# Kernel tuning notes

Hardware: AMD Instinct MI355X
Metric: run time of the kernel (lower is better)

Reference implementation:

```python
import jax, jax.numpy as jnp
import numpy as np

B, S, D = 8, 2048, 256


def setup_inputs() -> dict:
    key = jax.random.key(0)
    ks = jax.random.split(key, 8)
    nodes = jax.random.normal(ks[0], (B, S, D), dtype=jnp.float32)
    mask = jax.random.randint(ks[1], (B, S), 0, 2, dtype=jnp.int32)
    # ensure at least one unmasked position per row to avoid all--inf softmax
    mask = mask.at[:, 0].set(1)
    scale = 1.0 / np.sqrt(D)
    Wq = jax.random.normal(ks[2], (D, D), dtype=jnp.float32) * scale
    bq = jnp.zeros((D,), dtype=jnp.float32)
    Wk = jax.random.normal(ks[3], (D, D), dtype=jnp.float32) * scale
    bk = jnp.zeros((D,), dtype=jnp.float32)
    Wv = jax.random.normal(ks[4], (D, D), dtype=jnp.float32) * scale
    bv = jnp.zeros((D,), dtype=jnp.float32)
    return {"nodes": nodes, "mask": mask, "Wq": Wq, "bq": bq,
            "Wk": Wk, "bk": bk, "Wv": Wv, "bv": bv}


def reference(nodes, mask, Wq, bq, Wk, bk, Wv, bv):
    # Linear layers: x @ W.T + b (torch nn.Linear convention)
    q = jnp.einsum('bsd,ed->bse', nodes, Wq) + bq   # [B,S,D]
    k = jnp.einsum('bsd,ed->bse', nodes, Wk) + bk
    v = jnp.einsum('bsd,ed->bse', nodes, Wv) + bv
    d = k.shape[-1]
    scores = jnp.einsum('bqd,bkd->bqk', q, k) / jnp.sqrt(jnp.float32(d))  # [B,S,S]
    # mask[b, j] == 0 masks key column j for every query row
    scores = jnp.where(mask[:, None, :] != 0, scores, -jnp.inf)
    attn = jax.nn.softmax(scores, axis=-1)           # [B,S,S]
    weighted = jnp.einsum('bqk,bkd->bqd', attn, v)   # [B,S,D]
    return jnp.mean(weighted, axis=1)                # [B,D]
```

## Files before the change

### kernel.cpp

```cpp
#include <hip/hip_runtime.h>
#include <hip/hip_bf16.h>
#include <stdint.h>


typedef short short8 __attribute__((ext_vector_type(8)));
typedef float floatx4 __attribute__((ext_vector_type(4)));
typedef float floatx2 __attribute__((ext_vector_type(2)));

#define MFMA16(a, b, c) __builtin_amdgcn_mfma_f32_16x16x32_bf16((a), (b), (c), 0, 0, 0)

#define ASYNC16(gsrc, ldst)                                                    \
    __builtin_amdgcn_global_load_lds(                                          \
        (__attribute__((address_space(1))) void*)(void*)(gsrc),                \
        (__attribute__((address_space(3))) void*)(ldst), 16, 0, 0)

static __device__ __forceinline__ unsigned short f2bf(float f) {
    union { float f; unsigned u; } v; v.f = f;
    unsigned r = v.u + 0x7fffu + ((v.u >> 16) & 1u);
    return (unsigned short)(r >> 16);
}
static __device__ __forceinline__ float bf2f(unsigned short h) {
    union { unsigned u; float f; } v; v.u = ((unsigned)h) << 16;
    return v.f;
}

__global__ __launch_bounds__(256) void k_cc(
    const float* __restrict__ nodes, const float* __restrict__ Wq,
    const float* __restrict__ Wk, const float* __restrict__ Wv,
    unsigned short* __restrict__ nbf, unsigned short* __restrict__ wbf,
    const int* __restrict__ mask, int* __restrict__ cidx, int* __restrict__ cnt,
    int* __restrict__ slot_of ,
    unsigned short* __restrict__ kbt,
    float* __restrict__ zbase ,
    float* __restrict__ outp )
{
    int blk = blockIdx.x;
    if (blk < 2144) {
        int unit = blk * 256 + threadIdx.x;
        const float* src;
        unsigned short* dst;
        int off;
        if (unit < 524288) {
            src = nodes; dst = nbf; off = unit * 8;
        } else {
            int j = (unit - 524288) * 8;
            int m = j >> 16;
            int r = j & 65535;
            src = (m == 0) ? Wq : (m == 1 ? Wk : Wv);
            dst = wbf + m * 65536;
            off = r;
        }
        float4 a = *(const float4*)(src + off);
        float4 b = *(const float4*)(src + off + 4);
        short8 o;
        o[0] = f2bf(a.x); o[1] = f2bf(a.y); o[2] = f2bf(a.z); o[3] = f2bf(a.w);
        o[4] = f2bf(b.x); o[5] = f2bf(b.y); o[6] = f2bf(b.z); o[7] = f2bf(b.w);
        *(short8*)(dst + off) = o;
        return;
    }
    if (blk < 2152) {
        if (threadIdx.x < 64) {
            int b = blk - 2144, lane = threadIdx.x;
            int base = 0;
            for (int c = 0; c < 2048; c += 64) {
                int m = mask[b * 2048 + c + lane];
                unsigned long long bal = __ballot(m != 0);
                int pre = __popcll(bal & ((1ull << lane) - 1ull));
                if (m) {
                    cidx[b * 2048 + base + pre] = c + lane;
                    slot_of[b * 2048 + c + lane] = base + pre;
                } else {
                    slot_of[b * 2048 + c + lane] = -1;
                }
                base += __popcll(bal);
            }
            if (lane == 0) cnt[b] = base;
            for (int i = base + lane; i < 2048; i += 64) cidx[b * 2048 + i] = 0;
            int cntPad = (base + 63) & ~63;
            int pad = cntPad - base;
            short8 z8 = {};
            for (int i = lane; i < pad * 32; i += 64) {
                int slot = base + (i >> 5);
                int du = i & 31;
                size_t off = ((size_t)b * 32 + (slot >> 6)) * 16384
                           + ((size_t)du * 64 + (slot & 63)) * 8;
                *(short8*)(kbt + off) = z8;
            }
        }
        return;
    }
    int idx = (blk - 2152) * 256 + threadIdx.x;
    float4 z = {0.f, 0.f, 0.f, 0.f};
#pragma unroll
    for (int j = 0; j < 2; ++j) {
        int p = idx + j * 4352;
        if (p < 8192) ((float4*)zbase)[p] = z;
        else ((float4*)outp)[p - 8192] = z;
    }
}

__global__ __launch_bounds__(256) void k_proj2b(
    const unsigned short* __restrict__ nbf,
    const unsigned short* __restrict__ wbf,
    const float* __restrict__ bq, const float* __restrict__ bk,
    const float* __restrict__ bv,
    const int* __restrict__ slot_of,
    unsigned short* __restrict__ qb, unsigned short* __restrict__ kbt,
    unsigned short* __restrict__ vb)
{
    __shared__ __align__(16) unsigned short As[128 * 64];
    __shared__ __align__(16) unsigned short Bs[128 * 64];
    int tid = threadIdx.x, lane = tid & 63, wave = tid >> 6;
    int wm = wave & 1, wn = wave >> 1;
    int l15 = lane & 15, quad = lane >> 4;
    int mBase = blockIdx.x * 128;
    int nBase = blockIdx.y * 128;
    int z = blockIdx.z;
    const unsigned short* W = wbf + z * 65536;

    floatx4 acc[4][4] = {};

    for (int kc = 0; kc < 256; kc += 64) {
#pragma unroll
        for (int i = 0; i < 4; ++i) {
            int p = i * 256 + wave * 64 + lane;
            int row = p >> 3;
            int col8 = (p & 7) ^ (row & 7);
            int goff = row * 256 + kc + col8 * 8;
            unsigned short* dstA = &As[(i * 256 + wave * 64) * 8];
            unsigned short* dstB = &Bs[(i * 256 + wave * 64) * 8];
            ASYNC16(nbf + mBase * 256 + goff, dstA);
            ASYNC16(W + nBase * 256 + goff, dstB);
        }
        __syncthreads();
#pragma unroll
        for (int ks = 0; ks < 2; ++ks) {
            int c8 = ks * 4 + quad;
            short8 af[4], bfr[4];
#pragma unroll
            for (int i = 0; i < 4; ++i) {
                int row = wm * 64 + i * 16 + l15;
                af[i] = *(const short8*)(&As[(row * 8 + (c8 ^ (row & 7))) * 8]);
            }
#pragma unroll
            for (int i = 0; i < 4; ++i) {
                int row = wn * 64 + i * 16 + l15;
                bfr[i] = *(const short8*)(&Bs[(row * 8 + (c8 ^ (row & 7))) * 8]);
            }
#pragma unroll
            for (int mi = 0; mi < 4; ++mi)
#pragma unroll
                for (int ni = 0; ni < 4; ++ni)
                    acc[mi][ni] = MFMA16(af[mi], bfr[ni], acc[mi][ni]);
        }
        __syncthreads();
    }

    const float* bias = (z == 0) ? bq : (z == 1 ? bk : bv);
    float scale = (z == 0) ? 0.0625f : 1.0f;
    if (z == 1) {
#pragma unroll
        for (int mi = 0; mi < 4; ++mi)
#pragma unroll
            for (int ni = 0; ni < 4; ++ni) {
                int col = nBase + wn * 64 + ni * 16 + l15;
                float bval = bias[col];
                int du = col >> 3, cj = col & 7;
#pragma unroll
                for (int r = 0; r < 4; ++r) {
                    int row = mBase + wm * 64 + mi * 16 + quad * 4 + r;
                    int slot = slot_of[row];
                    if (slot >= 0) {
                        int b = row >> 11;
                        size_t off = ((size_t)b * 32 + (slot >> 6)) * 16384
                                   + ((size_t)du * 64 + (slot & 63)) * 8 + cj;
                        kbt[off] = f2bf(acc[mi][ni][r] + bval);
                    }
                }
            }
    } else {
        unsigned short* out = (z == 0) ? qb : vb;
#pragma unroll
        for (int mi = 0; mi < 4; ++mi)
#pragma unroll
            for (int ni = 0; ni < 4; ++ni) {
                int col = nBase + wn * 64 + ni * 16 + l15;
                float bval = bias[col];
#pragma unroll
                for (int r = 0; r < 4; ++r) {
                    int row = mBase + wm * 64 + mi * 16 + quad * 4 + r;
                    out[row * 256 + col] = f2bf((acc[mi][ni][r] + bval) * scale);
                }
            }
    }
}

__global__ __launch_bounds__(256) void k_pass1v(
    const unsigned short* __restrict__ qb, const unsigned short* __restrict__ kbt,
    const int* __restrict__ cnt_g, float* __restrict__ lsum_g,
    unsigned char* __restrict__ pbuf)
{
    __shared__ __align__(16) unsigned short kt[16384];
    int tid = threadIdx.x, lane = tid & 63, wave = tid >> 6;
    int l15 = lane & 15, quad = lane >> 4;
    int b = blockIdx.z;
    int cnt = cnt_g[b];
    int nchunk = (cnt + 63) >> 6;
    int qBase = blockIdx.x * 128 + wave * 32;
    int qcg = blockIdx.x * 4 + wave;

    short8 qf[2][8];
#pragma unroll
    for (int mi = 0; mi < 2; ++mi)
#pragma unroll
        for (int ks = 0; ks < 8; ++ks)
            qf[mi][ks] = *(const short8*)(qb + (b * 2048 + qBase + mi * 16 + l15) * 256 + ks * 32 + quad * 8);

    float ls[2][4] = {};
    for (int c = blockIdx.y; c < nchunk; c += 4) {
        const unsigned short* src = kbt + ((size_t)b * 32 + c) * 16384;
#pragma unroll
        for (int i = 0; i < 8; ++i) {
            int seg = wave * 8 + i;
            ASYNC16(src + seg * 512 + lane * 8, &kt[seg * 512]);
        }
        __syncthreads();
#pragma unroll
        for (int nt = 0; nt < 4; ++nt) {
            short8 kf[8];
#pragma unroll
            for (int ks = 0; ks < 8; ++ks)
                kf[ks] = *(const short8*)(&kt[((ks * 4 + quad) * 64 + nt * 16 + l15) * 8]);
            floatx4 acc[2] = {};
#pragma unroll
            for (int ks = 0; ks < 8; ++ks) {
                acc[0] = MFMA16(qf[0][ks], kf[ks], acc[0]);
                acc[1] = MFMA16(qf[1][ks], kf[ks], acc[1]);
            }
            float bias = (c * 64 + nt * 16 + l15 < cnt) ? 0.0f : -1e30f;
            float e[2][4];
#pragma unroll
            for (int mi = 0; mi < 2; ++mi)
#pragma unroll
                for (int r = 0; r < 4; ++r) {
                    e[mi][r] = __expf(acc[mi][r] + bias);
                    ls[mi][r] += e[mi][r];
                }
            int ktile = c * 4 + nt;
            if (ktile < 96) {
                int w0 = __builtin_amdgcn_cvt_pk_fp8_f32(e[0][0], e[0][1], 0, 0);
                w0 = __builtin_amdgcn_cvt_pk_fp8_f32(e[0][2], e[0][3], w0, 1);
                int w1 = __builtin_amdgcn_cvt_pk_fp8_f32(e[1][0], e[1][1], 0, 0);
                w1 = __builtin_amdgcn_cvt_pk_fp8_f32(e[1][2], e[1][3], w1, 1);
                size_t off = ((((size_t)b * 96 + ktile) * 64 + qcg) * 64 + lane) * 8;
                uint2 pv; pv.x = (unsigned)w0; pv.y = (unsigned)w1;
                *(uint2*)(pbuf + off) = pv;
            }
        }
        __syncthreads();
    }
#pragma unroll
    for (int mi = 0; mi < 2; ++mi)
#pragma unroll
        for (int r = 0; r < 4; ++r) {
            float v = ls[mi][r];
            v += __shfl_xor(v, 1); v += __shfl_xor(v, 2);
            v += __shfl_xor(v, 4); v += __shfl_xor(v, 8);
            if (l15 == 0)
                atomicAdd(&lsum_g[b * 2048 + qBase + mi * 16 + quad * 4 + r], v);
        }
}

__global__ __launch_bounds__(512) void k_wred5(
    const unsigned char* __restrict__ pbuf, const float* __restrict__ lsum_g,
    const int* __restrict__ cidx, const int* __restrict__ cnt_g,
    float* __restrict__ wsum_g)
{
    __shared__ float linv_p[2048];
    int tid = threadIdx.x, lane = tid & 63, wave = tid >> 6;
    int l15 = lane & 15, quad = lane >> 4;
    int b = blockIdx.z;
    int ktile = blockIdx.y * 8 + wave;

#pragma unroll
    for (int i = 0; i < 4; ++i) {
        int idx = i * 512 + tid;
        int qcg = idx >> 5, qd = (idx >> 3) & 3, j = idx & 7;
        int q = qcg * 32 + (j >> 2) * 16 + qd * 4 + (j & 3);
        linv_p[idx] = 1.0f / lsum_g[b * 2048 + q];
    }
    __syncthreads();

    int cnt = cnt_g[b];
    if (ktile >= 96 || ktile * 16 >= cnt) return;

    int qcg0 = blockIdx.x * 32;
    float acc = 0.f;
#pragma unroll 4
    for (int qcg = qcg0; qcg < qcg0 + 32; ++qcg) {
        size_t off = ((((size_t)b * 96 + ktile) * 64 + qcg) * 64 + lane) * 8;
        uint2 pv = *(const uint2*)(pbuf + off);
        const float* lv = &linv_p[(qcg * 4 + quad) * 8];
        floatx2 p01 = __builtin_amdgcn_cvt_pk_f32_fp8(pv.x, 0);
        floatx2 p23 = __builtin_amdgcn_cvt_pk_f32_fp8(pv.x, 1);
        floatx2 p45 = __builtin_amdgcn_cvt_pk_f32_fp8(pv.y, 0);
        floatx2 p67 = __builtin_amdgcn_cvt_pk_f32_fp8(pv.y, 1);
        acc += p01[0] * lv[0] + p01[1] * lv[1] + p23[0] * lv[2] + p23[1] * lv[3]
             + p45[0] * lv[4] + p45[1] * lv[5] + p67[0] * lv[6] + p67[1] * lv[7];
    }
    acc += __shfl_xor(acc, 16);
    acc += __shfl_xor(acc, 32);
    int slot = ktile * 16 + l15;
    if (lane < 16 && slot < cnt)
        atomicAdd(&wsum_g[b * 2048 + cidx[b * 2048 + slot]], acc);
}

__global__ __launch_bounds__(256) void k_out(
    const float* __restrict__ wsum_g, const unsigned short* __restrict__ vb,
    float* __restrict__ outp)
{
    int b = blockIdx.y;
    int d = threadIdx.x;
    int k0 = blockIdx.x * 128;
    float acc = 0.f;
#pragma unroll 4
    for (int k = k0; k < k0 + 128; ++k) {
        float wv = wsum_g[b * 2048 + k];
        acc += wv * bf2f(vb[(b * 2048 + k) * 256 + d]);
    }
    atomicAdd(&outp[b * 256 + d], acc * (1.0f / 2048.0f));
}

extern "C" void kernel_launch(void* const* d_in, const int* in_sizes, int n_in,
                              void* d_out, int out_size, void* d_ws, size_t ws_size,
                              hipStream_t stream)
{
    const float* nodes = (const float*)d_in[0];
    const int*   mask  = (const int*)d_in[1];
    const float* Wq    = (const float*)d_in[2];
    const float* bq    = (const float*)d_in[3];
    const float* Wk    = (const float*)d_in[4];
    const float* bk    = (const float*)d_in[5];
    const float* Wv    = (const float*)d_in[6];
    const float* bv    = (const float*)d_in[7];
    float* out = (float*)d_out;

    unsigned short* qb  = (unsigned short*)d_ws;
    unsigned short* vb  = qb + 4194304;
    float* lsum = (float*)(vb + 4194304);
    float* wsum = lsum + 16384;
    int*   cnt  = (int*)(wsum + 16384);
    int*   cidx = cnt + 16;
    int*   slot_of = cidx + 16384;
    unsigned short* kbt = (unsigned short*)(slot_of + 16384);
    unsigned short* X   = kbt + 4194304;
    unsigned short* nbf = X;
    unsigned short* wbf = X + 4194304;
    unsigned char* pbuf = (unsigned char*)X;

    k_cc<<<2169, 256, 0, stream>>>(nodes, Wq, Wk, Wv, nbf, wbf,
                                   mask, cidx, cnt, slot_of, kbt, lsum, out);
    k_proj2b<<<dim3(128, 2, 3), 256, 0, stream>>>(nbf, wbf, bq, bk, bv,
                                                  slot_of, qb, kbt, vb);
    k_pass1v<<<dim3(16, 4, 8), 256, 0, stream>>>(qb, kbt, cnt, lsum, pbuf);
    k_wred5<<<dim3(2, 16, 8), 512, 0, stream>>>(pbuf, lsum, cidx, cnt, wsum);
    k_out<<<dim3(16, 8), 256, 0, stream>>>(wsum, vb, out);
}
```

Baseline: 140.8 us.

## Fuse weight reduction and V-weighted output into a single kernel

Merges the softmax-weight column reduction kernel with the final V-weighted sum kernel. Each block now covers 64 compacted key slots across all query groups, keeps the per-key weights in shared memory, and multiplies them directly against the V rows via cidx. This removes one launch, the wsum global atomics and their round trip. Only unmasked keys are touched, so V reads drop to roughly half. The cost is fewer, larger blocks (256 instead of 256 blocks of differing shape) with less parallelism per block in the reduction phase.

```diff
diff --git a/kernel.cpp b/kernel.cpp
--- a/kernel.cpp
+++ b/kernel.cpp
@@ -271,16 +271,21 @@
         }
 }
 
-__global__ __launch_bounds__(512) void k_wred5(
+__global__ __launch_bounds__(512) void k_wredout(
     const unsigned char* __restrict__ pbuf, const float* __restrict__ lsum_g,
     const int* __restrict__ cidx, const int* __restrict__ cnt_g,
-    float* __restrict__ wsum_g)
+    const unsigned short* __restrict__ vb, float* __restrict__ outp)
 {
     __shared__ float linv_p[2048];
+    __shared__ float wsh[2][64];
     int tid = threadIdx.x, lane = tid & 63, wave = tid >> 6;
     int l15 = lane & 15, quad = lane >> 4;
-    int b = blockIdx.z;
-    int ktile = blockIdx.y * 8 + wave;
+    int b = blockIdx.y;
+    int cnt = cnt_g[b];
+    if (blockIdx.x * 64 >= cnt) return;
+
+    int ktile = blockIdx.x * 4 + (wave >> 1);
+    int qhalf = wave & 1;
 
 #pragma unroll
     for (int i = 0; i < 4; ++i) {
@@ -291,44 +296,44 @@
     }
     __syncthreads();
 
-    int cnt = cnt_g[b];
-    if (ktile >= 96 || ktile * 16 >= cnt) return;
-
-    int qcg0 = blockIdx.x * 32;
     float acc = 0.f;
+    if (ktile < 96 && ktile * 16 < cnt) {
+        int qcg0 = qhalf * 32;
 #pragma unroll 4
-    for (int qcg = qcg0; qcg < qcg0 + 32; ++qcg) {
-        size_t off = ((((size_t)b * 96 + ktile) * 64 + qcg) * 64 + lane) * 8;
-        uint2 pv = *(const uint2*)(pbuf + off);
-        const float* lv = &linv_p[(qcg * 4 + quad) * 8];
-        floatx2 p01 = __builtin_amdgcn_cvt_pk_f32_fp8(pv.x, 0);
-        floatx2 p23 = __builtin_amdgcn_cvt_pk_f32_fp8(pv.x, 1);
-        floatx2 p45 = __builtin_amdgcn_cvt_pk_f32_fp8(pv.y, 0);
-        floatx2 p67 = __builtin_amdgcn_cvt_pk_f32_fp8(pv.y, 1);
-        acc += p01[0] * lv[0] + p01[1] * lv[1] + p23[0] * lv[2] + p23[1] * lv[3]
-             + p45[0] * lv[4] + p45[1] * lv[5] + p67[0] * lv[6] + p67[1] * lv[7];
-    }
-    acc += __shfl_xor(acc, 16);
-    acc += __shfl_xor(acc, 32);
-    int slot = ktile * 16 + l15;
-    if (lane < 16 && slot < cnt)
-        atomicAdd(&wsum_g[b * 2048 + cidx[b * 2048 + slot]], acc);
-}
-
-__global__ __launch_bounds__(256) void k_out(
-    const float* __restrict__ wsum_g, const unsigned short* __restrict__ vb,
-    float* __restrict__ outp)
-{
-    int b = blockIdx.y;
-    int d = threadIdx.x;
-    int k0 = blockIdx.x * 128;
-    float acc = 0.f;
+        for (int qcg = qcg0; qcg < qcg0 + 32; ++qcg) {
+            size_t off = ((((size_t)b * 96 + ktile) * 64 + qcg) * 64 + lane) * 8;
+            uint2 pv = *(const uint2*)(pbuf + off);
+            const float* lv = &linv_p[(qcg * 4 + quad) * 8];
+            floatx2 p01 = __builtin_amdgcn_cvt_pk_f32_fp8(pv.x, 0);
+            floatx2 p23 = __builtin_amdgcn_cvt_pk_f32_fp8(pv.x, 1);
+            floatx2 p45 = __builtin_amdgcn_cvt_pk_f32_fp8(pv.y, 0);
+            floatx2 p67 = __builtin_amdgcn_cvt_pk_f32_fp8(pv.y, 1);
+            acc += p01[0] * lv[0] + p01[1] * lv[1] + p23[0] * lv[2] + p23[1] * lv[3]
+                 + p45[0] * lv[4] + p45[1] * lv[5] + p67[0] * lv[6] + p67[1] * lv[7];
+        }
+        acc += __shfl_xor(acc, 16);
+        acc += __shfl_xor(acc, 32);
+    }
+    if (lane < 16) {
+        int local = (wave >> 1) * 16 + l15;
+        bool ok = (ktile < 96) && (ktile * 16 + l15 < cnt);
+        wsh[qhalf][local] = ok ? acc : 0.f;
+    }
+    __syncthreads();
+
+    int d = tid & 255, g = tid >> 8;
+    float oacc = 0.f;
 #pragma unroll 4
-    for (int k = k0; k < k0 + 128; ++k) {
-        float wv = wsum_g[b * 2048 + k];
-        acc += wv * bf2f(vb[(b * 2048 + k) * 256 + d]);
-    }
-    atomicAdd(&outp[b * 256 + d], acc * (1.0f / 2048.0f));
+    for (int j = 0; j < 32; ++j) {
+        int local = g * 32 + j;
+        int slot = blockIdx.x * 64 + local;
+        float w = wsh[0][local] + wsh[1][local];
+        if (slot < cnt && w != 0.f) {
+            int key = cidx[b * 2048 + slot];
+            oacc += w * bf2f(vb[(b * 2048 + key) * 256 + d]);
+        }
+    }
+    atomicAdd(&outp[b * 256 + d], oacc * (1.0f / 2048.0f));
 }
 
 extern "C" void kernel_launch(void* const* d_in, const int* in_sizes, int n_in,
@@ -363,6 +368,5 @@
     k_proj2b<<<dim3(128, 2, 3), 256, 0, stream>>>(nbf, wbf, bq, bk, bv,
                                                   slot_of, qb, kbt, vb);
     k_pass1v<<<dim3(16, 4, 8), 256, 0, stream>>>(qb, kbt, cnt, lsum, pbuf);
-    k_wred5<<<dim3(2, 16, 8), 512, 0, stream>>>(pbuf, lsum, cidx, cnt, wsum);
-    k_out<<<dim3(16, 8), 256, 0, stream>>>(wsum, vb, out);
-}
+    k_wredout<<<dim3(32, 8), 512, 0, stream>>>(pbuf, lsum, cidx, cnt, vb, out);
+}
```

Result: slower. 148.9 us (+5.8%).
